# Optimization experiments

Hardware: AMD Instinct MI355X
Metric: run time of the kernel (lower is better)

## Reference

```python
import jax, jax.numpy as jnp
import numpy as np

N, E, NFEAT, H = 100000, 1600000, 128, 128
NLAYER = 3


def setup_inputs() -> dict:
    key = jax.random.key(0)
    ks = jax.random.split(key, 20)
    s = 0.05
    return {
        "features": jax.random.normal(ks[0], (N, NFEAT), jnp.float32),
        "edge_index": jax.random.randint(ks[1], (2, E), 0, N, jnp.int32),
        "edge_weight": jax.random.uniform(ks[2], (E,), jnp.float32),
        "w1": jax.random.normal(ks[3], (H, NFEAT), jnp.float32) * s,
        "b1": jnp.zeros((H,), jnp.float32),
        "gin_w1": jax.random.normal(ks[4], (NLAYER, H, H), jnp.float32) * s,
        "gin_b1": jnp.zeros((NLAYER, H), jnp.float32),
        "gin_w2": jax.random.normal(ks[5], (NLAYER, H, H), jnp.float32) * s,
        "gin_b2": jnp.zeros((NLAYER, H), jnp.float32),
        "gru_wih": jax.random.normal(ks[6], (NLAYER, 3 * H, H), jnp.float32) * s,
        "gru_whh": jax.random.normal(ks[7], (NLAYER, 3 * H, H), jnp.float32) * s,
        "gru_bih": jnp.zeros((NLAYER, 3 * H), jnp.float32),
        "gru_bhh": jnp.zeros((NLAYER, 3 * H), jnp.float32),
        "head_w1": jax.random.normal(ks[8], (NLAYER, H, H), jnp.float32) * s,
        "head_b1": jnp.zeros((NLAYER, H), jnp.float32),
        "head_w2_0": jax.random.normal(ks[9], (2, H), jnp.float32) * s,
        "head_b2_0": jnp.zeros((2,), jnp.float32),
        "head_w2_1": jax.random.normal(ks[10], (6, H), jnp.float32) * s,
        "head_b2_1": jnp.zeros((6,), jnp.float32),
        "head_w2_2": jax.random.normal(ks[11], (21, H), jnp.float32) * s,
        "head_b2_2": jnp.zeros((21,), jnp.float32),
    }


def _gru_cell(x, h, wih, whh, bih, bhh):
    # torch.nn.GRUCell semantics
    gi = x @ wih.T + bih           # [N, 3H]
    gh = h @ whh.T + bhh           # [N, 3H]
    ir, iz, inn = jnp.split(gi, 3, axis=1)
    hr, hz, hn = jnp.split(gh, 3, axis=1)
    r = jax.nn.sigmoid(ir + hr)
    z = jax.nn.sigmoid(iz + hz)
    n = jnp.tanh(inn + r * hn)
    return (1.0 - z) * n + z * h


def reference(features, edge_index, edge_weight, w1, b1,
              gin_w1, gin_b1, gin_w2, gin_b2,
              gru_wih, gru_whh, gru_bih, gru_bhh,
              head_w1, head_b1,
              head_w2_0, head_b2_0, head_w2_1, head_b2_1, head_w2_2, head_b2_2):
    n_nodes = features.shape[0]
    dst, src = edge_index[0], edge_index[1]  # spmm: out[dst] += w * x[src]
    head_w2 = [head_w2_0, head_w2_1, head_w2_2]
    head_b2 = [head_b2_0, head_b2_1, head_b2_2]

    x = jax.nn.relu(features @ w1.T + b1)  # mlp1 + ReLU
    layer_info = x
    outputs, _outputs = [], []
    for i in range(NLAYER):
        agg = jax.ops.segment_sum(edge_weight[:, None] * x[src], dst,
                                  num_segments=n_nodes)
        h = _gru_cell(agg, layer_info, gru_wih[i], gru_whh[i],
                      gru_bih[i], gru_bhh[i])
        # GinMlp: Linear -> ReLU -> Linear, then outer ReLU
        x = jax.nn.relu(h @ gin_w1[i].T + gin_b1[i]) @ gin_w2[i].T + gin_b2[i]
        x = jax.nn.relu(x)
        # custom layer-norm variant
        x = x / jnp.sqrt(1.0 + jnp.sum(x * x, axis=1, keepdims=True))
        # prediction head for this layer (mlpPos = [0,1,2])
        tmp = jax.nn.relu(x @ head_w1[i].T + head_b1[i]) @ head_w2[i].T + head_b2[i]
        outputs.append(jax.nn.log_softmax(tmp, axis=1))
        _outputs.append(jax.nn.softmax(tmp, axis=1))
        layer_info = x
    return tuple(outputs) + tuple(_outputs)
```

## Files before the change

kernel.cpp:

```cpp
#include <hip/hip_runtime.h>
#include <cstdint>
#include <cstddef>


typedef short  v8s __attribute__((ext_vector_type(8)));
typedef float  v4f __attribute__((ext_vector_type(4)));

#define BUCKET_CAP 4096

static __device__ __forceinline__ float bf2f(uint16_t u) {
  return __uint_as_float(((uint32_t)u) << 16);
}
static __device__ __forceinline__ uint16_t f2b(float f) {
  uint32_t x = __float_as_uint(f);
  return (uint16_t)((x + 0x7FFFu + ((x >> 16) & 1u)) >> 16);
}
static __device__ __forceinline__ float sigmoidf_(float v) {
  return 1.f / (1.f + __expf(-v));
}
static __device__ __forceinline__ float tanhf_(float v) {
  return 1.f - 2.f / (__expf(2.f * v) + 1.f);
}

__global__ void k_detect(const uint32_t* __restrict__ u, int* __restrict__ flag) {
  int lane = threadIdx.x;
  uint32_t low = u[lane] & 0xFFFFu;
  uint32_t e = (low >> 7) & 0xFFu;
  bool pass = (e == 0) || (e >= 110 && e <= 141);
  unsigned long long b = __ballot(pass);
  if (lane == 0) *flag = (__popcll(b) >= 32) ? 1 : 0;
}

struct CvtDesc {
  const void* src[18];
  int off[19];
};

__global__ void k_cvtw(CvtDesc c, float* __restrict__ wbase,
                       uint16_t* __restrict__ wb16,
                       const int* __restrict__ flag, int total) {
  int gid = blockIdx.x * 256 + threadIdx.x;
  if (gid >= total) return;
  int t = 0;
#pragma unroll
  for (int i = 1; i < 18; i++)
    if (gid >= c.off[i]) t = i;
  int local = gid - c.off[t];
  float v;
  if (*flag) v = bf2f(((const uint16_t*)c.src[t])[local]);
  else       v = ((const float*)c.src[t])[local];
  wbase[gid] = v;
  wb16[gid] = f2b(v);
}

__global__ void k_cvt_feat(const void* __restrict__ src, uint16_t* __restrict__ dst,
                           int n, const int* __restrict__ flag) {
  int i = blockIdx.x * 256 + threadIdx.x;
  if (i >= n) return;
  if (*flag) dst[i] = ((const uint16_t*)src)[i];
  else       dst[i] = f2b(((const float*)src)[i]);
}

__global__ void k_zero_i(int* __restrict__ p, int n) {
  int i = blockIdx.x * 256 + threadIdx.x;
  if (i < n) p[i] = 0;
}

__global__ void k_zero_f(float* __restrict__ p, int n) {
  int i = blockIdx.x * 256 + threadIdx.x;
  if (i < n) p[i] = 0.f;
}

__global__ void k_pack_mm(const uint16_t* __restrict__ src, uint16_t* __restrict__ dst,
                          int nmat) {
  int id = blockIdx.x * 256 + threadIdx.x;
  if (id >= nmat * 2048) return;
  int mat = id >> 11;
  int rem = id & 2047;
  int blk = rem >> 6, lane = rem & 63;
  int kc = blk >> 3, t = blk & 7;
  int n0 = lane & 15, quad = lane >> 4;
  const uint16_t* s = src + (size_t)mat * 16384 + (size_t)(t * 16 + n0) * 128 + kc * 32 + quad * 8;
  uint16_t* d = dst + (size_t)id * 8;
  *reinterpret_cast<v8s*>(d) = *reinterpret_cast<const v8s*>(s);
}

__global__ void k_pack_gru(const uint16_t* __restrict__ wih, const uint16_t* __restrict__ whh,
                           uint16_t* __restrict__ dst, int nlayer) {
  int id = blockIdx.x * 256 + threadIdx.x;
  if (id >= nlayer * 192 * 64) return;
  int lane = id & 63;
  int blk = (id >> 6) % 192;
  int layer = (id >> 6) / 192;
  int g = blk % 3;
  int mat = (blk / 3) % 2;
  int u = (blk / 6) % 2;
  int w = (blk / 12) % 4;
  int kc = blk / 48;
  int n0 = lane & 15, quad = lane >> 4;
  const uint16_t* base = (mat == 0 ? wih : whh) + (size_t)layer * 384 * 128;
  const uint16_t* s = base + (size_t)(g * 128 + w * 32 + u * 16 + n0) * 128 + kc * 32 + quad * 8;
  uint16_t* d = dst + ((size_t)layer * 192 + blk) * 512 + (size_t)lane * 8;
  *reinterpret_cast<v8s*>(d) = *reinterpret_cast<const v8s*>(s);
}

__global__ void k_part(const int* __restrict__ dst, const int* __restrict__ src,
                       const void* __restrict__ w, int* __restrict__ gcur,
                       uint2* __restrict__ ep0, const int* __restrict__ flag,
                       int E, int NB) {
  __shared__ int hist[1024];
  __shared__ int lbase[1024];
  int t = threadIdx.x;
  int CH = (E + gridDim.x - 1) / gridDim.x;
  int e0 = blockIdx.x * CH;
  int e1 = e0 + CH;
  if (e1 > E) e1 = E;
  for (int b = t; b < NB; b += 256) hist[b] = 0;
  __syncthreads();
  for (int e = e0 + t; e < e1; e += 256)
    atomicAdd(&hist[dst[e] >> 7], 1);
  __syncthreads();
  for (int b = t; b < NB; b += 256) {
    int c = hist[b];
    lbase[b] = c ? atomicAdd(&gcur[b], c) : 0;
    hist[b] = 0;
  }
  __syncthreads();
  bool bf = (*flag) != 0;
  for (int e = e0 + t; e < e1; e += 256) {
    int d = dst[e];
    int b = d >> 7;
    int pos = lbase[b] + atomicAdd(&hist[b], 1);
    if (pos >= BUCKET_CAP) pos = BUCKET_CAP - 1;
    float wv = bf ? bf2f(((const uint16_t*)w)[e]) : ((const float*)w)[e];
    ep0[(size_t)b * BUCKET_CAP + pos] =
        make_uint2((uint32_t)src[e] | (((uint32_t)d & 127u) << 25),
                   __float_as_uint(wv));
  }
}

__global__ void k_bprefix(const int* __restrict__ gcur, int* __restrict__ bbase,
                          int nbuckets) {
  __shared__ int red[256];
  int t = threadIdx.x;
  int chunk = (nbuckets + 255) >> 8;
  int beg = t * chunk;
  int end = beg + chunk;
  if (end > nbuckets) end = nbuckets;
  int s = 0;
  for (int b = beg; b < end; b++) {
    int c = gcur[b];
    if (c > BUCKET_CAP) c = BUCKET_CAP;
    bbase[b] = c;
    s += c;
  }
  red[t] = s;
  __syncthreads();
  for (int off = 1; off < 256; off <<= 1) {
    int u = (t >= off) ? red[t - off] : 0;
    __syncthreads();
    red[t] += u;
    __syncthreads();
  }
  int run = red[t] - s;
  for (int b = beg; b < end; b++) {
    int tot = bbase[b];
    bbase[b] = run;
    run += tot;
  }
}

__global__ void k_build(const uint2* __restrict__ ep0, const int* __restrict__ gcur,
                        const int* __restrict__ bbase, int* __restrict__ rowptr,
                        uint2* __restrict__ ep, int n, int nbuckets) {
  __shared__ int lcnt[128];
  __shared__ int lsc[128];
  int b = blockIdx.x, t = threadIdx.x;
  int cnt = gcur[b];
  if (cnt > BUCKET_CAP) cnt = BUCKET_CAP;
  if (t < 128) lcnt[t] = 0;
  __syncthreads();

  const uint2* sp = ep0 + (size_t)b * BUCKET_CAP;
  for (int p = t; p < cnt; p += 256)
    atomicAdd(&lcnt[sp[p].x >> 25], 1);
  __syncthreads();

  if (t < 128) lsc[t] = lcnt[t];
  __syncthreads();
  for (int off = 1; off < 128; off <<= 1) {
    int v = 0;
    if (t < 128 && t >= off) v = lsc[t - off];
    __syncthreads();
    if (t < 128) lsc[t] += v;
    __syncthreads();
  }

  int base = bbase[b];
  if (t < 128) {
    int excl = lsc[t] - lcnt[t];
    int node = b * 128 + t;
    if (node < n) rowptr[node] = base + excl;
    lcnt[t] = base + excl;
  }
  if (b == nbuckets - 1 && t == 0) rowptr[n] = base + lsc[127];
  __syncthreads();

  for (int p = t; p < cnt; p += 256) {
    uint2 v = sp[p];
    int pos = atomicAdd(&lcnt[v.x >> 25], 1);
    ep[pos] = make_uint2(v.x & 0x01FFFFFFu, v.y);
  }
}

__global__ void k_spmm(const uint16_t* __restrict__ x, const int* __restrict__ rowptr,
                       const uint2* __restrict__ ep, uint16_t* __restrict__ agg, int n) {
  int node = blockIdx.x * 4 + (threadIdx.x >> 6);
  int lane = threadIdx.x & 63;
  if (node >= n) return;
  int p0 = rowptr[node], p1 = rowptr[node + 1];
  float a0 = 0.f, a1 = 0.f;
  int p = p0;
  for (; p + 3 < p1; p += 4) {
    uint2 e0 = ep[p], e1 = ep[p + 1], e2 = ep[p + 2], e3 = ep[p + 3];
    uint32_t u0 = *reinterpret_cast<const uint32_t*>(x + (size_t)e0.x * 128 + lane * 2);
    uint32_t u1 = *reinterpret_cast<const uint32_t*>(x + (size_t)e1.x * 128 + lane * 2);
    uint32_t u2 = *reinterpret_cast<const uint32_t*>(x + (size_t)e2.x * 128 + lane * 2);
    uint32_t u3 = *reinterpret_cast<const uint32_t*>(x + (size_t)e3.x * 128 + lane * 2);
    float w0 = __uint_as_float(e0.y), w1 = __uint_as_float(e1.y);
    float w2 = __uint_as_float(e2.y), w3 = __uint_as_float(e3.y);
    a0 = fmaf(w0, bf2f((uint16_t)u0), a0);
    a1 = fmaf(w0, bf2f((uint16_t)(u0 >> 16)), a1);
    a0 = fmaf(w1, bf2f((uint16_t)u1), a0);
    a1 = fmaf(w1, bf2f((uint16_t)(u1 >> 16)), a1);
    a0 = fmaf(w2, bf2f((uint16_t)u2), a0);
    a1 = fmaf(w2, bf2f((uint16_t)(u2 >> 16)), a1);
    a0 = fmaf(w3, bf2f((uint16_t)u3), a0);
    a1 = fmaf(w3, bf2f((uint16_t)(u3 >> 16)), a1);
  }
  for (; p < p1; p++) {
    uint2 e0 = ep[p];
    float w0 = __uint_as_float(e0.y);
    uint32_t u0 = *reinterpret_cast<const uint32_t*>(x + (size_t)e0.x * 128 + lane * 2);
    a0 = fmaf(w0, bf2f((uint16_t)u0), a0);
    a1 = fmaf(w0, bf2f((uint16_t)(u0 >> 16)), a1);
  }
  uint32_t packed = (uint32_t)f2b(a0) | ((uint32_t)f2b(a1) << 16);
  *reinterpret_cast<uint32_t*>(agg + (size_t)node * 128 + lane * 2) = packed;
}

template <int EPI>
__launch_bounds__(256)
__global__ void k_mm(const uint16_t* __restrict__ A, const uint16_t* __restrict__ Wrp,
                     const float* __restrict__ bias, uint16_t* __restrict__ C,
                     int nrows) {
  int wave = threadIdx.x >> 6, lane = threadIdx.x & 63;
  int n0 = lane & 15, quad = lane >> 4;
  int m0 = (blockIdx.x * 4 + wave) * 32;
  int r0 = m0 + n0, r1 = m0 + 16 + n0;
  bool ok0 = r0 < nrows, ok1 = r1 < nrows;
  const v8s z8 = {0, 0, 0, 0, 0, 0, 0, 0};

  v4f acc[2][8];
#pragma unroll
  for (int rt = 0; rt < 2; rt++)
#pragma unroll
    for (int t = 0; t < 8; t++) acc[rt][t] = {0.f, 0.f, 0.f, 0.f};

  const uint16_t* ap0 = A + (size_t)r0 * 128 + quad * 8;
  const uint16_t* ap1 = A + (size_t)r1 * 128 + quad * 8;
#pragma unroll
  for (int kc = 0; kc < 4; kc++) {
    v8s a0 = ok0 ? *reinterpret_cast<const v8s*>(ap0 + kc * 32) : z8;
    v8s a1 = ok1 ? *reinterpret_cast<const v8s*>(ap1 + kc * 32) : z8;
    const uint16_t* wp = Wrp + (size_t)kc * 4096 + (size_t)lane * 8;
#pragma unroll
    for (int t = 0; t < 8; t++) {
      v8s bf = *reinterpret_cast<const v8s*>(wp + t * 512);
      acc[0][t] = __builtin_amdgcn_mfma_f32_16x16x32_bf16(a0, bf, acc[0][t], 0, 0, 0);
      acc[1][t] = __builtin_amdgcn_mfma_f32_16x16x32_bf16(a1, bf, acc[1][t], 0, 0, 0);
    }
  }

#pragma unroll
  for (int rt = 0; rt < 2; rt++) {
    int mb = m0 + rt * 16;
    float vv[8][4];
#pragma unroll
    for (int t = 0; t < 8; t++) {
      float b = bias[t * 16 + n0];
#pragma unroll
      for (int r = 0; r < 4; r++) vv[t][r] = fmaxf(acc[rt][t][r] + b, 0.f);
    }
    if (EPI == 2) {
#pragma unroll
      for (int r = 0; r < 4; r++) {
        float ss = 0.f;
#pragma unroll
        for (int t = 0; t < 8; t++) ss = fmaf(vv[t][r], vv[t][r], ss);
        ss += __shfl_xor(ss, 1);
        ss += __shfl_xor(ss, 2);
        ss += __shfl_xor(ss, 4);
        ss += __shfl_xor(ss, 8);
        float sc = rsqrtf(1.f + ss);
#pragma unroll
        for (int t = 0; t < 8; t++) vv[t][r] *= sc;
      }
    }
#pragma unroll
    for (int r = 0; r < 4; r++) {
      int row = mb + quad * 4 + r;
      if (row >= nrows) continue;
#pragma unroll
      for (int t = 0; t < 8; t++)
        C[(size_t)row * 128 + t * 16 + n0] = f2b(vv[t][r]);
    }
  }
}

__launch_bounds__(256)
__global__ void k_mm12(const uint16_t* __restrict__ A, const uint16_t* __restrict__ W1rp,
                       const float* __restrict__ b1, const uint16_t* __restrict__ W2rp,
                       const float* __restrict__ b2, uint16_t* __restrict__ C,
                       int nrows) {
  __shared__ uint16_t hl[128][136];
  int wave = threadIdx.x >> 6, lane = threadIdx.x & 63;
  int n0 = lane & 15, quad = lane >> 4;
  int m0 = (blockIdx.x * 4 + wave) * 32;
  int r0 = m0 + n0, r1 = m0 + 16 + n0;
  bool ok0 = r0 < nrows, ok1 = r1 < nrows;
  const v8s z8 = {0, 0, 0, 0, 0, 0, 0, 0};

  v4f acc[2][8];
#pragma unroll
  for (int rt = 0; rt < 2; rt++)
#pragma unroll
    for (int t = 0; t < 8; t++) acc[rt][t] = {0.f, 0.f, 0.f, 0.f};

  const uint16_t* ap0 = A + (size_t)r0 * 128 + quad * 8;
  const uint16_t* ap1 = A + (size_t)r1 * 128 + quad * 8;
#pragma unroll
  for (int kc = 0; kc < 4; kc++) {
    v8s a0 = ok0 ? *reinterpret_cast<const v8s*>(ap0 + kc * 32) : z8;
    v8s a1 = ok1 ? *reinterpret_cast<const v8s*>(ap1 + kc * 32) : z8;
    const uint16_t* wp = W1rp + (size_t)kc * 4096 + (size_t)lane * 8;
#pragma unroll
    for (int t = 0; t < 8; t++) {
      v8s bf = *reinterpret_cast<const v8s*>(wp + t * 512);
      acc[0][t] = __builtin_amdgcn_mfma_f32_16x16x32_bf16(a0, bf, acc[0][t], 0, 0, 0);
      acc[1][t] = __builtin_amdgcn_mfma_f32_16x16x32_bf16(a1, bf, acc[1][t], 0, 0, 0);
    }
  }

#pragma unroll
  for (int rt = 0; rt < 2; rt++) {
#pragma unroll
    for (int t = 0; t < 8; t++) {
      float b = b1[t * 16 + n0];
#pragma unroll
      for (int r = 0; r < 4; r++) {
        int rl = wave * 32 + rt * 16 + quad * 4 + r;
        hl[rl][t * 16 + n0] = f2b(fmaxf(acc[rt][t][r] + b, 0.f));
      }
    }
  }
  __syncthreads();

  v4f acc2[2][8];
#pragma unroll
  for (int rt = 0; rt < 2; rt++)
#pragma unroll
    for (int t = 0; t < 8; t++) acc2[rt][t] = {0.f, 0.f, 0.f, 0.f};

#pragma unroll
  for (int kc = 0; kc < 4; kc++) {
    v8s a0 = *reinterpret_cast<const v8s*>(&hl[wave * 32 + n0][kc * 32 + quad * 8]);
    v8s a1 = *reinterpret_cast<const v8s*>(&hl[wave * 32 + 16 + n0][kc * 32 + quad * 8]);
    const uint16_t* wp = W2rp + (size_t)kc * 4096 + (size_t)lane * 8;
#pragma unroll
    for (int t = 0; t < 8; t++) {
      v8s bf = *reinterpret_cast<const v8s*>(wp + t * 512);
      acc2[0][t] = __builtin_amdgcn_mfma_f32_16x16x32_bf16(a0, bf, acc2[0][t], 0, 0, 0);
      acc2[1][t] = __builtin_amdgcn_mfma_f32_16x16x32_bf16(a1, bf, acc2[1][t], 0, 0, 0);
    }
  }

#pragma unroll
  for (int rt = 0; rt < 2; rt++) {
    int mb = m0 + rt * 16;
    float vv[8][4];
#pragma unroll
    for (int t = 0; t < 8; t++) {
      float b = b2[t * 16 + n0];
#pragma unroll
      for (int r = 0; r < 4; r++) vv[t][r] = fmaxf(acc2[rt][t][r] + b, 0.f);
    }
#pragma unroll
    for (int r = 0; r < 4; r++) {
      float ss = 0.f;
#pragma unroll
      for (int t = 0; t < 8; t++) ss = fmaf(vv[t][r], vv[t][r], ss);
      ss += __shfl_xor(ss, 1);
      ss += __shfl_xor(ss, 2);
      ss += __shfl_xor(ss, 4);
      ss += __shfl_xor(ss, 8);
      float sc = rsqrtf(1.f + ss);
#pragma unroll
      for (int t = 0; t < 8; t++) vv[t][r] *= sc;
    }
#pragma unroll
    for (int r = 0; r < 4; r++) {
      int row = mb + quad * 4 + r;
      if (row >= nrows) continue;
#pragma unroll
      for (int t = 0; t < 8; t++)
        C[(size_t)row * 128 + t * 16 + n0] = f2b(vv[t][r]);
    }
  }
}

__launch_bounds__(512, 2)
__global__ void k_gru8(const uint16_t* __restrict__ agg, const uint16_t* __restrict__ xb,
                       const uint16_t* __restrict__ Wrp,
                       const float* __restrict__ bih, const float* __restrict__ bhh,
                       uint16_t* __restrict__ hb, int n, int ntiles) {
  int wave = threadIdx.x >> 6, lane = threadIdx.x & 63;
  int n0 = lane & 15, quad = lane >> 4;
  int s = wave >> 1, u = wave & 1;
  const v8s z8 = {0, 0, 0, 0, 0, 0, 0, 0};

  v8s wf[24];
#pragma unroll
  for (int kc = 0; kc < 4; kc++)
#pragma unroll
    for (int mat = 0; mat < 2; mat++)
#pragma unroll
      for (int g = 0; g < 3; g++)
        wf[kc * 6 + mat * 3 + g] = *reinterpret_cast<const v8s*>(
            Wrp + (size_t)((kc * 4 + s) * 12 + (u * 2 + mat) * 3 + g) * 512 +
            (size_t)lane * 8);

  int col = wave * 16 + n0;
  float bir = bih[col], biz = bih[128 + col], bin = bih[256 + col];
  float bhr = bhh[col], bhz = bhh[128 + col], bhn = bhh[256 + col];

  for (int tt = blockIdx.x; tt < ntiles; tt += gridDim.x) {
    int m0 = tt * 32;
    int r0 = m0 + n0, r1 = m0 + 16 + n0;
    bool ok0 = r0 < n, ok1 = r1 < n;

    v4f accI[2][3], accH[2][3];
#pragma unroll
    for (int rt = 0; rt < 2; rt++)
#pragma unroll
      for (int g = 0; g < 3; g++) {
        accI[rt][g] = {0.f, 0.f, 0.f, 0.f};
        accH[rt][g] = {0.f, 0.f, 0.f, 0.f};
      }

    const uint16_t* ap0 = agg + (size_t)r0 * 128 + quad * 8;
    const uint16_t* ap1 = agg + (size_t)r1 * 128 + quad * 8;
    const uint16_t* xp0 = xb + (size_t)r0 * 128 + quad * 8;
    const uint16_t* xp1 = xb + (size_t)r1 * 128 + quad * 8;
#pragma unroll
    for (int kc = 0; kc < 4; kc++) {
      v8s a0 = ok0 ? *reinterpret_cast<const v8s*>(ap0 + kc * 32) : z8;
      v8s a1 = ok1 ? *reinterpret_cast<const v8s*>(ap1 + kc * 32) : z8;
      v8s x0 = ok0 ? *reinterpret_cast<const v8s*>(xp0 + kc * 32) : z8;
      v8s x1 = ok1 ? *reinterpret_cast<const v8s*>(xp1 + kc * 32) : z8;
#pragma unroll
      for (int g = 0; g < 3; g++) {
        accI[0][g] = __builtin_amdgcn_mfma_f32_16x16x32_bf16(a0, wf[kc * 6 + g], accI[0][g], 0, 0, 0);
        accI[1][g] = __builtin_amdgcn_mfma_f32_16x16x32_bf16(a1, wf[kc * 6 + g], accI[1][g], 0, 0, 0);
        accH[0][g] = __builtin_amdgcn_mfma_f32_16x16x32_bf16(x0, wf[kc * 6 + 3 + g], accH[0][g], 0, 0, 0);
        accH[1][g] = __builtin_amdgcn_mfma_f32_16x16x32_bf16(x1, wf[kc * 6 + 3 + g], accH[1][g], 0, 0, 0);
      }
    }

#pragma unroll
    for (int rt = 0; rt < 2; rt++) {
#pragma unroll
      for (int r = 0; r < 4; r++) {
        int row = m0 + rt * 16 + quad * 4 + r;
        if (row < n) {
          float ir = accI[rt][0][r] + bir;
          float iz = accI[rt][1][r] + biz;
          float in_ = accI[rt][2][r] + bin;
          float hr = accH[rt][0][r] + bhr;
          float hz = accH[rt][1][r] + bhz;
          float hn = accH[rt][2][r] + bhn;
          float rr = sigmoidf_(ir + hr);
          float zz = sigmoidf_(iz + hz);
          float nn = tanhf_(fmaf(rr, hn, in_));
          float xv = bf2f(xb[(size_t)row * 128 + col]);
          hb[(size_t)row * 128 + col] = f2b(fmaf(zz, xv - nn, nn));
        }
      }
    }
  }
}

template <int C>
__launch_bounds__(256)
__global__ void k_mmh(const uint16_t* __restrict__ A, const uint16_t* __restrict__ Wrp,
                      const float* __restrict__ bias,
                      const float* __restrict__ w2, const float* __restrict__ b2,
                      float* __restrict__ out_log, float* __restrict__ out_soft,
                      int nrows) {
  __shared__ uint16_t hl[128][130];
  int wave = threadIdx.x >> 6, lane = threadIdx.x & 63;
  int n0 = lane & 15, quad = lane >> 4;
  int m0 = (blockIdx.x * 4 + wave) * 32;
  int r0 = m0 + n0, r1 = m0 + 16 + n0;
  bool ok0 = r0 < nrows, ok1 = r1 < nrows;
  const v8s z8 = {0, 0, 0, 0, 0, 0, 0, 0};

  v4f acc[2][8];
#pragma unroll
  for (int rt = 0; rt < 2; rt++)
#pragma unroll
    for (int t = 0; t < 8; t++) acc[rt][t] = {0.f, 0.f, 0.f, 0.f};

  const uint16_t* ap0 = A + (size_t)r0 * 128 + quad * 8;
  const uint16_t* ap1 = A + (size_t)r1 * 128 + quad * 8;
#pragma unroll
  for (int kc = 0; kc < 4; kc++) {
    v8s a0 = ok0 ? *reinterpret_cast<const v8s*>(ap0 + kc * 32) : z8;
    v8s a1 = ok1 ? *reinterpret_cast<const v8s*>(ap1 + kc * 32) : z8;
    const uint16_t* wp = Wrp + (size_t)kc * 4096 + (size_t)lane * 8;
#pragma unroll
    for (int t = 0; t < 8; t++) {
      v8s bf = *reinterpret_cast<const v8s*>(wp + t * 512);
      acc[0][t] = __builtin_amdgcn_mfma_f32_16x16x32_bf16(a0, bf, acc[0][t], 0, 0, 0);
      acc[1][t] = __builtin_amdgcn_mfma_f32_16x16x32_bf16(a1, bf, acc[1][t], 0, 0, 0);
    }
  }

#pragma unroll
  for (int rt = 0; rt < 2; rt++) {
#pragma unroll
    for (int t = 0; t < 8; t++) {
      float b = bias[t * 16 + n0];
#pragma unroll
      for (int r = 0; r < 4; r++) {
        int rl = wave * 32 + rt * 16 + quad * 4 + r;
        hl[rl][t * 16 + n0] = f2b(fmaxf(acc[rt][t][r] + b, 0.f));
      }
    }
  }
  __syncthreads();

  int tid = threadIdx.x;
  if (tid < 128) {
    int node = blockIdx.x * 128 + tid;
    if (node < nrows) {
      float lg[C];
#pragma unroll
      for (int c = 0; c < C; c++) lg[c] = b2[c];
      for (int k = 0; k < 64; k++) {
        uint32_t u = *reinterpret_cast<const uint32_t*>(&hl[tid][2 * k]);
        float x0 = bf2f((uint16_t)u);
        float x1 = bf2f((uint16_t)(u >> 16));
#pragma unroll
        for (int c = 0; c < C; c++) lg[c] = fmaf(x0, w2[c * 128 + 2 * k], lg[c]);
#pragma unroll
        for (int c = 0; c < C; c++) lg[c] = fmaf(x1, w2[c * 128 + 2 * k + 1], lg[c]);
      }
      float m = lg[0];
#pragma unroll
      for (int c = 1; c < C; c++) m = fmaxf(m, lg[c]);
      float sum = 0.f;
      float e[C];
#pragma unroll
      for (int c = 0; c < C; c++) { e[c] = __expf(lg[c] - m); sum += e[c]; }
      float ls = __logf(sum);
      float inv = 1.f / sum;
#pragma unroll
      for (int c = 0; c < C; c++) {
        out_log[(size_t)node * C + c] = lg[c] - m - ls;
        out_soft[(size_t)node * C + c] = e[c] * inv;
      }
    }
  }
}

extern "C" void kernel_launch(void* const* d_in, const int* in_sizes, int n_in,
                              void* d_out, int out_size, void* d_ws, size_t ws_size,
                              hipStream_t stream) {
  const int N = in_sizes[0] / 128;
  const int E = in_sizes[2];
  const int NB = (N + 127) >> 7;

  static const int wn[18] = {16384, 128, 49152, 384, 49152, 384,
                             147456, 147456, 1152, 1152, 49152, 384,
                             256, 2, 768, 6, 2688, 21};
  CvtDesc cd;
  int off = 0;
  for (int i = 0; i < 18; i++) {
    cd.src[i] = d_in[3 + i];
    cd.off[i] = off;
    off += wn[i];
  }
  cd.off[18] = off;
  const int wtotal = off;

  char* p = (char*)d_ws;
  size_t used = 0;
  auto alloc = [&](size_t bytes) -> char* {
    char* r = p;
    size_t b = (bytes + 255) & ~(size_t)255;
    p += b;
    used += b;
    return r;
  };
  int*      flag    = (int*)alloc(256);
  float*    wbase   = (float*)alloc((size_t)wtotal * 4);
  uint16_t* wb16    = (uint16_t*)alloc((size_t)wtotal * 2);
  uint16_t* mmrp    = (uint16_t*)alloc((size_t)10 * 16384 * 2);
  uint16_t* grurp   = (uint16_t*)alloc((size_t)3 * 192 * 512 * 2);
  uint16_t* xb      = (uint16_t*)alloc((size_t)N * 128 * 2);
  uint16_t* aggb    = (uint16_t*)alloc((size_t)N * 128 * 2);
  uint16_t* hb      = (uint16_t*)alloc((size_t)N * 128 * 2);
  int*      rowptr  = (int*)alloc((size_t)(N + 1) * 4);
  int*      gcur    = (int*)alloc((size_t)NB * 4);
  int*      bbase   = (int*)alloc((size_t)(NB + 1) * 4);
  uint2*    ep0     = (uint2*)alloc((size_t)NB * BUCKET_CAP * 8);
  uint2*    epack   = (uint2*)alloc((size_t)E * 8);

  float* out = (float*)d_out;
  float* outlog[3]  = {out, out + 2 * (size_t)N, out + 8 * (size_t)N};
  float* outsoft[3] = {out + 29 * (size_t)N, out + 31 * (size_t)N, out + 37 * (size_t)N};

  if (used > ws_size) {
    k_zero_f<<<(out_size + 255) / 256, 256, 0, stream>>>(out, out_size);
    return;
  }

  float* b1f   = wbase + cd.off[1];
  float* ginb1 = wbase + cd.off[3];
  float* ginb2 = wbase + cd.off[5];
  float* bih   = wbase + cd.off[8];
  float* bhh   = wbase + cd.off[9];
  float* hb1   = wbase + cd.off[11];
  float* hw2_0 = wbase + cd.off[12];
  float* hb2_0 = wbase + cd.off[13];
  float* hw2_1 = wbase + cd.off[14];
  float* hb2_1 = wbase + cd.off[15];
  float* hw2_2 = wbase + cd.off[16];
  float* hb2_2 = wbase + cd.off[17];

  uint16_t* w1b   = wb16 + cd.off[0];
  uint16_t* ginw1b= wb16 + cd.off[2];
  uint16_t* ginw2b= wb16 + cd.off[4];
  uint16_t* wihb  = wb16 + cd.off[6];
  uint16_t* whhb  = wb16 + cd.off[7];
  uint16_t* hw1b  = wb16 + cd.off[10];

  uint16_t* w1rp    = mmrp;
  uint16_t* ginw1rp = mmrp + (size_t)1 * 16384;
  uint16_t* ginw2rp = mmrp + (size_t)4 * 16384;
  uint16_t* hw1rp   = mmrp + (size_t)7 * 16384;

  const int* dst = (const int*)d_in[1];
  const int* src = (const int*)d_in[1] + E;

  k_detect<<<1, 64, 0, stream>>>((const uint32_t*)d_in[0], flag);
  k_cvtw<<<(wtotal + 255) / 256, 256, 0, stream>>>(cd, wbase, wb16, flag, wtotal);
  k_cvt_feat<<<((size_t)N * 128 + 255) / 256, 256, 0, stream>>>(d_in[0], aggb,
                                                                N * 128, flag);
  k_pack_mm<<<(1 * 2048 + 255) / 256, 256, 0, stream>>>(w1b, w1rp, 1);
  k_pack_mm<<<(3 * 2048 + 255) / 256, 256, 0, stream>>>(ginw1b, ginw1rp, 3);
  k_pack_mm<<<(3 * 2048 + 255) / 256, 256, 0, stream>>>(ginw2b, ginw2rp, 3);
  k_pack_mm<<<(3 * 2048 + 255) / 256, 256, 0, stream>>>(hw1b, hw1rp, 3);
  k_pack_gru<<<(3 * 192 * 64 + 255) / 256, 256, 0, stream>>>(wihb, whhb, grurp, 3);

  k_zero_i<<<(NB + 255) / 256, 256, 0, stream>>>(gcur, NB);
  k_part<<<256, 256, 0, stream>>>(dst, src, d_in[2], gcur, ep0, flag, E, NB);
  k_bprefix<<<1, 256, 0, stream>>>(gcur, bbase, NB);
  k_build<<<NB, 256, 0, stream>>>(ep0, gcur, bbase, rowptr, epack, N, NB);

  int mmrb = (N + 127) / 128;
  int spb  = (N + 3) / 4;
  int ntiles32 = (N + 31) / 32;

  k_mm<1><<<mmrb, 256, 0, stream>>>(aggb, w1rp, b1f, xb, N);

  for (int i = 0; i < 3; i++) {
    k_spmm<<<spb, 256, 0, stream>>>(xb, rowptr, epack, aggb, N);
    k_gru8<<<256, 512, 0, stream>>>(aggb, xb, grurp + (size_t)i * 192 * 512,
                                    bih + i * 384, bhh + i * 384, hb, N, ntiles32);
    k_mm12<<<mmrb, 256, 0, stream>>>(hb, ginw1rp + (size_t)i * 16384,
                                     ginb1 + i * 128,
                                     ginw2rp + (size_t)i * 16384,
                                     ginb2 + i * 128, xb, N);
    if (i == 0)
      k_mmh<2><<<mmrb, 256, 0, stream>>>(xb, hw1rp, hb1, hw2_0, hb2_0,
                                         outlog[0], outsoft[0], N);
    else if (i == 1)
      k_mmh<6><<<mmrb, 256, 0, stream>>>(xb, hw1rp + (size_t)16384, hb1 + 128,
                                         hw2_1, hb2_1, outlog[1], outsoft[1], N);
    else
      k_mmh<21><<<mmrb, 256, 0, stream>>>(xb, hw1rp + (size_t)2 * 16384, hb1 + 256,
                                          hw2_2, hb2_2, outlog[2], outsoft[2], N);
  }
}
```

Baseline: 829.7 us.

## Fuse GIN MLP with prediction head and split SpMM edges across half-waves

The GIN two-layer MLP kernel now also runs the per-layer prediction head (MFMA matmul, ReLU, small projection, log-softmax/softmax) on the normalized tile kept in shared memory. This removes a separate head kernel launch and its re-read of x. SpMM now gives each half-wave alternate edges, with each lane loading 4 bf16 features, and combines the halves with a cross-lane shuffle. Edge records are read with nontemporal loads. The fused kernel needs extra barriers and more registers, which may lower occupancy.

```diff
diff --git a/kernel.cpp b/kernel.cpp
--- a/kernel.cpp
+++ b/kernel.cpp
@@ -218,35 +218,62 @@
   int node = blockIdx.x * 4 + (threadIdx.x >> 6);
   int lane = threadIdx.x & 63;
   if (node >= n) return;
+  int half = lane >> 5;
+  int l32 = lane & 31;
   int p0 = rowptr[node], p1 = rowptr[node + 1];
-  float a0 = 0.f, a1 = 0.f;
-  int p = p0;
-  for (; p + 3 < p1; p += 4) {
-    uint2 e0 = ep[p], e1 = ep[p + 1], e2 = ep[p + 2], e3 = ep[p + 3];
-    uint32_t u0 = *reinterpret_cast<const uint32_t*>(x + (size_t)e0.x * 128 + lane * 2);
-    uint32_t u1 = *reinterpret_cast<const uint32_t*>(x + (size_t)e1.x * 128 + lane * 2);
-    uint32_t u2 = *reinterpret_cast<const uint32_t*>(x + (size_t)e2.x * 128 + lane * 2);
-    uint32_t u3 = *reinterpret_cast<const uint32_t*>(x + (size_t)e3.x * 128 + lane * 2);
-    float w0 = __uint_as_float(e0.y), w1 = __uint_as_float(e1.y);
-    float w2 = __uint_as_float(e2.y), w3 = __uint_as_float(e3.y);
-    a0 = fmaf(w0, bf2f((uint16_t)u0), a0);
-    a1 = fmaf(w0, bf2f((uint16_t)(u0 >> 16)), a1);
-    a0 = fmaf(w1, bf2f((uint16_t)u1), a0);
-    a1 = fmaf(w1, bf2f((uint16_t)(u1 >> 16)), a1);
-    a0 = fmaf(w2, bf2f((uint16_t)u2), a0);
-    a1 = fmaf(w2, bf2f((uint16_t)(u2 >> 16)), a1);
-    a0 = fmaf(w3, bf2f((uint16_t)u3), a0);
-    a1 = fmaf(w3, bf2f((uint16_t)(u3 >> 16)), a1);
-  }
-  for (; p < p1; p++) {
-    uint2 e0 = ep[p];
-    float w0 = __uint_as_float(e0.y);
-    uint32_t u0 = *reinterpret_cast<const uint32_t*>(x + (size_t)e0.x * 128 + lane * 2);
-    a0 = fmaf(w0, bf2f((uint16_t)u0), a0);
-    a1 = fmaf(w0, bf2f((uint16_t)(u0 >> 16)), a1);
-  }
-  uint32_t packed = (uint32_t)f2b(a0) | ((uint32_t)f2b(a1) << 16);
-  *reinterpret_cast<uint32_t*>(agg + (size_t)node * 128 + lane * 2) = packed;
+  float a0 = 0.f, a1 = 0.f, a2 = 0.f, a3 = 0.f;
+  const uint16_t* xc = x + (size_t)l32 * 4;
+  const uint64_t* ep64 = reinterpret_cast<const uint64_t*>(ep);
+  int p = p0 + half;
+  for (; p + 6 < p1; p += 8) {
+    uint64_t e0 = __builtin_nontemporal_load(&ep64[p]);
+    uint64_t e1 = __builtin_nontemporal_load(&ep64[p + 2]);
+    uint64_t e2 = __builtin_nontemporal_load(&ep64[p + 4]);
+    uint64_t e3 = __builtin_nontemporal_load(&ep64[p + 6]);
+    uint2 r0 = *reinterpret_cast<const uint2*>(xc + (size_t)(uint32_t)e0 * 128);
+    uint2 r1 = *reinterpret_cast<const uint2*>(xc + (size_t)(uint32_t)e1 * 128);
+    uint2 r2 = *reinterpret_cast<const uint2*>(xc + (size_t)(uint32_t)e2 * 128);
+    uint2 r3 = *reinterpret_cast<const uint2*>(xc + (size_t)(uint32_t)e3 * 128);
+    float w0 = __uint_as_float((uint32_t)(e0 >> 32));
+    float w1 = __uint_as_float((uint32_t)(e1 >> 32));
+    float w2 = __uint_as_float((uint32_t)(e2 >> 32));
+    float w3 = __uint_as_float((uint32_t)(e3 >> 32));
+    a0 = fmaf(w0, bf2f((uint16_t)r0.x), a0);
+    a1 = fmaf(w0, bf2f((uint16_t)(r0.x >> 16)), a1);
+    a2 = fmaf(w0, bf2f((uint16_t)r0.y), a2);
+    a3 = fmaf(w0, bf2f((uint16_t)(r0.y >> 16)), a3);
+    a0 = fmaf(w1, bf2f((uint16_t)r1.x), a0);
+    a1 = fmaf(w1, bf2f((uint16_t)(r1.x >> 16)), a1);
+    a2 = fmaf(w1, bf2f((uint16_t)r1.y), a2);
+    a3 = fmaf(w1, bf2f((uint16_t)(r1.y >> 16)), a3);
+    a0 = fmaf(w2, bf2f((uint16_t)r2.x), a0);
+    a1 = fmaf(w2, bf2f((uint16_t)(r2.x >> 16)), a1);
+    a2 = fmaf(w2, bf2f((uint16_t)r2.y), a2);
+    a3 = fmaf(w2, bf2f((uint16_t)(r2.y >> 16)), a3);
+    a0 = fmaf(w3, bf2f((uint16_t)r3.x), a0);
+    a1 = fmaf(w3, bf2f((uint16_t)(r3.x >> 16)), a1);
+    a2 = fmaf(w3, bf2f((uint16_t)r3.y), a2);
+    a3 = fmaf(w3, bf2f((uint16_t)(r3.y >> 16)), a3);
+  }
+  for (; p < p1; p += 2) {
+    uint64_t e0 = __builtin_nontemporal_load(&ep64[p]);
+    uint2 r0 = *reinterpret_cast<const uint2*>(xc + (size_t)(uint32_t)e0 * 128);
+    float w0 = __uint_as_float((uint32_t)(e0 >> 32));
+    a0 = fmaf(w0, bf2f((uint16_t)r0.x), a0);
+    a1 = fmaf(w0, bf2f((uint16_t)(r0.x >> 16)), a1);
+    a2 = fmaf(w0, bf2f((uint16_t)r0.y), a2);
+    a3 = fmaf(w0, bf2f((uint16_t)(r0.y >> 16)), a3);
+  }
+  a0 += __shfl_xor(a0, 32);
+  a1 += __shfl_xor(a1, 32);
+  a2 += __shfl_xor(a2, 32);
+  a3 += __shfl_xor(a3, 32);
+  if (half == 0) {
+    uint2 o;
+    o.x = (uint32_t)f2b(a0) | ((uint32_t)f2b(a1) << 16);
+    o.y = (uint32_t)f2b(a2) | ((uint32_t)f2b(a3) << 16);
+    *reinterpret_cast<uint2*>(agg + (size_t)node * 128 + l32 * 4) = o;
+  }
 }
 
 template <int EPI>
@@ -318,11 +345,16 @@
   }
 }
 
+template <int C>
 __launch_bounds__(256)
-__global__ void k_mm12(const uint16_t* __restrict__ A, const uint16_t* __restrict__ W1rp,
-                       const float* __restrict__ b1, const uint16_t* __restrict__ W2rp,
-                       const float* __restrict__ b2, uint16_t* __restrict__ C,
-                       int nrows) {
+__global__ void k_mm12h(const uint16_t* __restrict__ A,
+                        const uint16_t* __restrict__ W1rp, const float* __restrict__ b1,
+                        const uint16_t* __restrict__ W2rp, const float* __restrict__ b2,
+                        const uint16_t* __restrict__ Whrp, const float* __restrict__ bh,
+                        const float* __restrict__ w2, const float* __restrict__ b2h,
+                        uint16_t* __restrict__ xbout,
+                        float* __restrict__ out_log, float* __restrict__ out_soft,
+                        int nrows) {
   __shared__ uint16_t hl[128][136];
   int wave = threadIdx.x >> 6, lane = threadIdx.x & 63;
   int n0 = lane & 15, quad = lane >> 4;
@@ -351,7 +383,6 @@
       acc[1][t] = __builtin_amdgcn_mfma_f32_16x16x32_bf16(a1, bf, acc[1][t], 0, 0, 0);
     }
   }
-
 #pragma unroll
   for (int rt = 0; rt < 2; rt++) {
 #pragma unroll
@@ -371,7 +402,6 @@
   for (int rt = 0; rt < 2; rt++)
 #pragma unroll
     for (int t = 0; t < 8; t++) acc2[rt][t] = {0.f, 0.f, 0.f, 0.f};
-
 #pragma unroll
   for (int kc = 0; kc < 4; kc++) {
     v8s a0 = *reinterpret_cast<const v8s*>(&hl[wave * 32 + n0][kc * 32 + quad * 8]);
@@ -384,7 +414,7 @@
       acc2[1][t] = __builtin_amdgcn_mfma_f32_16x16x32_bf16(a1, bf, acc2[1][t], 0, 0, 0);
     }
   }
-
+  __syncthreads();
 #pragma unroll
   for (int rt = 0; rt < 2; rt++) {
     int mb = m0 + rt * 16;
@@ -411,10 +441,79 @@
 #pragma unroll
     for (int r = 0; r < 4; r++) {
       int row = mb + quad * 4 + r;
-      if (row >= nrows) continue;
-#pragma unroll
-      for (int t = 0; t < 8; t++)
-        C[(size_t)row * 128 + t * 16 + n0] = f2b(vv[t][r]);
+      int rl = wave * 32 + rt * 16 + quad * 4 + r;
+#pragma unroll
+      for (int t = 0; t < 8; t++) {
+        uint16_t hv = f2b(vv[t][r]);
+        hl[rl][t * 16 + n0] = hv;
+        if (row < nrows) xbout[(size_t)row * 128 + t * 16 + n0] = hv;
+      }
+    }
+  }
+  __syncthreads();
+
+  v4f acc3[2][8];
+#pragma unroll
+  for (int rt = 0; rt < 2; rt++)
+#pragma unroll
+    for (int t = 0; t < 8; t++) acc3[rt][t] = {0.f, 0.f, 0.f, 0.f};
+#pragma unroll
+  for (int kc = 0; kc < 4; kc++) {
+    v8s a0 = *reinterpret_cast<const v8s*>(&hl[wave * 32 + n0][kc * 32 + quad * 8]);
+    v8s a1 = *reinterpret_cast<const v8s*>(&hl[wave * 32 + 16 + n0][kc * 32 + quad * 8]);
+    const uint16_t* wp = Whrp + (size_t)kc * 4096 + (size_t)lane * 8;
+#pragma unroll
+    for (int t = 0; t < 8; t++) {
+      v8s bf = *reinterpret_cast<const v8s*>(wp + t * 512);
+      acc3[0][t] = __builtin_amdgcn_mfma_f32_16x16x32_bf16(a0, bf, acc3[0][t], 0, 0, 0);
+      acc3[1][t] = __builtin_amdgcn_mfma_f32_16x16x32_bf16(a1, bf, acc3[1][t], 0, 0, 0);
+    }
+  }
+  __syncthreads();
+#pragma unroll
+  for (int rt = 0; rt < 2; rt++) {
+#pragma unroll
+    for (int t = 0; t < 8; t++) {
+      float b = bh[t * 16 + n0];
+#pragma unroll
+      for (int r = 0; r < 4; r++) {
+        int rl = wave * 32 + rt * 16 + quad * 4 + r;
+        hl[rl][t * 16 + n0] = f2b(fmaxf(acc3[rt][t][r] + b, 0.f));
+      }
+    }
+  }
+  __syncthreads();
+
+  int tid = threadIdx.x;
+  if (tid < 128) {
+    int node = blockIdx.x * 128 + tid;
+    if (node < nrows) {
+      float lg[C];
+#pragma unroll
+      for (int c = 0; c < C; c++) lg[c] = b2h[c];
+      for (int k = 0; k < 64; k++) {
+        uint32_t u = *reinterpret_cast<const uint32_t*>(&hl[tid][2 * k]);
+        float x0 = bf2f((uint16_t)u);
+        float x1 = bf2f((uint16_t)(u >> 16));
+#pragma unroll
+        for (int c = 0; c < C; c++) lg[c] = fmaf(x0, w2[c * 128 + 2 * k], lg[c]);
+#pragma unroll
+        for (int c = 0; c < C; c++) lg[c] = fmaf(x1, w2[c * 128 + 2 * k + 1], lg[c]);
+      }
+      float m = lg[0];
+#pragma unroll
+      for (int c = 1; c < C; c++) m = fmaxf(m, lg[c]);
+      float sum = 0.f;
+      float e[C];
+#pragma unroll
+      for (int c = 0; c < C; c++) { e[c] = __expf(lg[c] - m); sum += e[c]; }
+      float ls = __logf(sum);
+      float inv = 1.f / sum;
+#pragma unroll
+      for (int c = 0; c < C; c++) {
+        out_log[(size_t)node * C + c] = lg[c] - m - ls;
+        out_soft[(size_t)node * C + c] = e[c] * inv;
+      }
     }
   }
 }
@@ -495,90 +594,6 @@
           float xv = bf2f(xb[(size_t)row * 128 + col]);
           hb[(size_t)row * 128 + col] = f2b(fmaf(zz, xv - nn, nn));
         }
-      }
-    }
-  }
-}
-
-template <int C>
-__launch_bounds__(256)
-__global__ void k_mmh(const uint16_t* __restrict__ A, const uint16_t* __restrict__ Wrp,
-                      const float* __restrict__ bias,
-                      const float* __restrict__ w2, const float* __restrict__ b2,
-                      float* __restrict__ out_log, float* __restrict__ out_soft,
-                      int nrows) {
-  __shared__ uint16_t hl[128][130];
-  int wave = threadIdx.x >> 6, lane = threadIdx.x & 63;
-  int n0 = lane & 15, quad = lane >> 4;
-  int m0 = (blockIdx.x * 4 + wave) * 32;
-  int r0 = m0 + n0, r1 = m0 + 16 + n0;
-  bool ok0 = r0 < nrows, ok1 = r1 < nrows;
-  const v8s z8 = {0, 0, 0, 0, 0, 0, 0, 0};
-
-  v4f acc[2][8];
-#pragma unroll
-  for (int rt = 0; rt < 2; rt++)
-#pragma unroll
-    for (int t = 0; t < 8; t++) acc[rt][t] = {0.f, 0.f, 0.f, 0.f};
-
-  const uint16_t* ap0 = A + (size_t)r0 * 128 + quad * 8;
-  const uint16_t* ap1 = A + (size_t)r1 * 128 + quad * 8;
-#pragma unroll
-  for (int kc = 0; kc < 4; kc++) {
-    v8s a0 = ok0 ? *reinterpret_cast<const v8s*>(ap0 + kc * 32) : z8;
-    v8s a1 = ok1 ? *reinterpret_cast<const v8s*>(ap1 + kc * 32) : z8;
-    const uint16_t* wp = Wrp + (size_t)kc * 4096 + (size_t)lane * 8;
-#pragma unroll
-    for (int t = 0; t < 8; t++) {
-      v8s bf = *reinterpret_cast<const v8s*>(wp + t * 512);
-      acc[0][t] = __builtin_amdgcn_mfma_f32_16x16x32_bf16(a0, bf, acc[0][t], 0, 0, 0);
-      acc[1][t] = __builtin_amdgcn_mfma_f32_16x16x32_bf16(a1, bf, acc[1][t], 0, 0, 0);
-    }
-  }
-
-#pragma unroll
-  for (int rt = 0; rt < 2; rt++) {
-#pragma unroll
-    for (int t = 0; t < 8; t++) {
-      float b = bias[t * 16 + n0];
-#pragma unroll
-      for (int r = 0; r < 4; r++) {
-        int rl = wave * 32 + rt * 16 + quad * 4 + r;
-        hl[rl][t * 16 + n0] = f2b(fmaxf(acc[rt][t][r] + b, 0.f));
-      }
-    }
-  }
-  __syncthreads();
-
-  int tid = threadIdx.x;
-  if (tid < 128) {
-    int node = blockIdx.x * 128 + tid;
-    if (node < nrows) {
-      float lg[C];
-#pragma unroll
-      for (int c = 0; c < C; c++) lg[c] = b2[c];
-      for (int k = 0; k < 64; k++) {
-        uint32_t u = *reinterpret_cast<const uint32_t*>(&hl[tid][2 * k]);
-        float x0 = bf2f((uint16_t)u);
-        float x1 = bf2f((uint16_t)(u >> 16));
-#pragma unroll
-        for (int c = 0; c < C; c++) lg[c] = fmaf(x0, w2[c * 128 + 2 * k], lg[c]);
-#pragma unroll
-        for (int c = 0; c < C; c++) lg[c] = fmaf(x1, w2[c * 128 + 2 * k + 1], lg[c]);
-      }
-      float m = lg[0];
-#pragma unroll
-      for (int c = 1; c < C; c++) m = fmaxf(m, lg[c]);
-      float sum = 0.f;
-      float e[C];
-#pragma unroll
-      for (int c = 0; c < C; c++) { e[c] = __expf(lg[c] - m); sum += e[c]; }
-      float ls = __logf(sum);
-      float inv = 1.f / sum;
-#pragma unroll
-      for (int c = 0; c < C; c++) {
-        out_log[(size_t)node * C + c] = lg[c] - m - ls;
-        out_soft[(size_t)node * C + c] = e[c] * inv;
       }
     }
   }
@@ -689,18 +704,29 @@
     k_spmm<<<spb, 256, 0, stream>>>(xb, rowptr, epack, aggb, N);
     k_gru8<<<256, 512, 0, stream>>>(aggb, xb, grurp + (size_t)i * 192 * 512,
                                     bih + i * 384, bhh + i * 384, hb, N, ntiles32);
-    k_mm12<<<mmrb, 256, 0, stream>>>(hb, ginw1rp + (size_t)i * 16384,
-                                     ginb1 + i * 128,
-                                     ginw2rp + (size_t)i * 16384,
-                                     ginb2 + i * 128, xb, N);
     if (i == 0)
-      k_mmh<2><<<mmrb, 256, 0, stream>>>(xb, hw1rp, hb1, hw2_0, hb2_0,
-                                         outlog[0], outsoft[0], N);
+      k_mm12h<2><<<mmrb, 256, 0, stream>>>(hb, ginw1rp + (size_t)i * 16384,
+                                           ginb1 + i * 128,
+                                           ginw2rp + (size_t)i * 16384,
+                                           ginb2 + i * 128,
+                                           hw1rp + (size_t)i * 16384, hb1 + i * 128,
+                                           hw2_0, hb2_0, xb,
+                                           outlog[0], outsoft[0], N);
     else if (i == 1)
-      k_mmh<6><<<mmrb, 256, 0, stream>>>(xb, hw1rp + (size_t)16384, hb1 + 128,
-                                         hw2_1, hb2_1, outlog[1], outsoft[1], N);
+      k_mm12h<6><<<mmrb, 256, 0, stream>>>(hb, ginw1rp + (size_t)i * 16384,
+                                           ginb1 + i * 128,
+                                           ginw2rp + (size_t)i * 16384,
+                                           ginb2 + i * 128,
+                                           hw1rp + (size_t)i * 16384, hb1 + i * 128,
+                                           hw2_1, hb2_1, xb,
+                                           outlog[1], outsoft[1], N);
     else
-      k_mmh<21><<<mmrb, 256, 0, stream>>>(xb, hw1rp + (size_t)2 * 16384, hb1 + 256,
-                                          hw2_2, hb2_2, outlog[2], outsoft[2], N);
-  }
-}
+      k_mm12h<21><<<mmrb, 256, 0, stream>>>(hb, ginw1rp + (size_t)i * 16384,
+                                            ginb1 + i * 128,
+                                            ginw2rp + (size_t)i * 16384,
+                                            ginb2 + i * 128,
+                                            hw1rp + (size_t)i * 16384, hb1 + i * 128,
+                                            hw2_2, hb2_2, xb,
+                                            outlog[2], outsoft[2], N);
+  }
+}
```

Result: slower. 863.8 us (+4.1%).
